# Performance work log

Hardware: AMD Instinct MI355X
Metric: run time of the kernel (lower is better)

## Reference

```python
import jax, jax.numpy as jnp
import numpy as np

EPS = 1e-6

def _ln(x, g, b):
    m = x.mean(-1, keepdims=True)
    v = jnp.var(x, axis=-1, keepdims=True)
    return (x - m) * jax.lax.rsqrt(v + EPS) * g + b

def _mha(x, qkv_w, out_w, out_b, heads, dh):
    # vit-style attention: Linear(dim, 3*heads*dh, bias=False), chunk into q,k,v
    B, N, _ = x.shape
    qkv = (x @ qkv_w).reshape(B, N, 3, heads, dh).transpose(2, 0, 3, 1, 4)
    q, k, v = qkv[0], qkv[1], qkv[2]                       # [B,H,N,dh]
    attn = jax.nn.softmax(jnp.einsum('bhid,bhjd->bhij', q, k) * (dh ** -0.5), axis=-1)
    o = jnp.einsum('bhij,bhjd->bhid', attn, v).transpose(0, 2, 1, 3).reshape(B, N, heads * dh)
    return o @ out_w + out_b

def _tx(x, p, heads, dh):
    # standard prenorm transformer stack, p = stacked per-layer params
    (l1g, l1b, qw, ow, ob, l2g, l2b, f1w, f1b, f2w, f2b, ng, nb) = p
    for i in range(l1g.shape[0]):
        x = x + _mha(_ln(x, l1g[i], l1b[i]), qw[i], ow[i], ob[i], heads, dh)
        h = _ln(x, l2g[i], l2b[i])
        x = x + jax.nn.gelu(h @ f1w[i] + f1b[i]) @ f2w[i] + f2b[i]
    return _ln(x, ng, nb)

def _ats(x, l1g, l1b, qkvw, qkvb, projw, projb, l2g, l2b, f1w, f1b, f2w, f2b):
    # ATS block: attention + CLS-significance-driven adaptive token resampling (gather)
    B, N, D = x.shape
    heads = 6
    dh = D // heads
    h = _ln(x, l1g, l1b)
    qkv = (h @ qkvw + qkvb).reshape(B, N, 3, heads, dh).transpose(2, 0, 3, 1, 4)
    q, k, v = qkv[0], qkv[1], qkv[2]
    attn = jax.nn.softmax(jnp.einsum('bhid,bhjd->bhij', q, k) * (dh ** -0.5), axis=-1)  # [B,H,N,N]
    y = jnp.einsum('bhij,bhjd->bhid', attn, v).transpose(0, 2, 1, 3).reshape(B, N, D)
    y = y @ projw + projb
    # significance score: cls attention * value norm (ATS, Fayyaz et al.)
    vn = jnp.linalg.norm(v, axis=-1)                        # [B,H,N]
    s = (attn[:, :, 0, 1:] * vn[:, :, 1:]).mean(axis=1)     # [B,N-1]
    s = s / (s.sum(-1, keepdims=True) + 1e-8)
    cdf = jnp.cumsum(s, axis=-1)                            # [B,N-1]
    # deterministic inverse-transform sampling of N-1 tokens
    u = (jnp.arange(N - 1, dtype=x.dtype) + 0.5) / (N - 1)
    idx = jax.vmap(lambda c: jnp.searchsorted(c, u))(cdf)
    idx = jnp.clip(idx, 0, N - 2) + 1                       # skip cls slot
    idx = jnp.concatenate([jnp.zeros((B, 1), idx.dtype), idx], axis=1)  # keep cls
    g = lambda a: jnp.take_along_axis(a, idx[:, :, None], axis=1)
    x = g(x) + g(y)
    h = _ln(x, l2g, l2b)
    return x + jax.nn.gelu(h @ f1w + f1b) @ f2w + f2b

def reference(x, patch_w, patch_b, pos_emb, space_token, temporal_token,
              s_ln1_g, s_ln1_b, s_qkv_w, s_out_w, s_out_b, s_ln2_g, s_ln2_b,
              s_fc1_w, s_fc1_b, s_fc2_w, s_fc2_b, s_norm_g, s_norm_b,
              t_ln1_g, t_ln1_b, t_qkv_w, t_out_w, t_out_b, t_ln2_g, t_ln2_b,
              t_fc1_w, t_fc1_b, t_fc2_w, t_fc2_b, t_norm_g, t_norm_b,
              a_ln1_g, a_ln1_b, a_qkv_w, a_qkv_b, a_proj_w, a_proj_b,
              a_ln2_g, a_ln2_b, a_fc1_w, a_fc1_b, a_fc2_w, a_fc2_b,
              final_g, final_b, h1_w, h1_b, h2_w, h2_b):
    B, T = x.shape[0], x.shape[1]
    BT, D, P, HP = B * T, 192, 16, 14
    # patch embedding (conv16s16 as unfold + linear), channel-major flattening
    xt = x.reshape(BT, 3, HP, P, HP, P).transpose(0, 2, 4, 1, 3, 5).reshape(BT, HP * HP, 3 * P * P)
    xt = (xt @ patch_w + patch_b).reshape(B, T, HP * HP, D)
    cls = jnp.broadcast_to(space_token.reshape(1, 1, 1, D), (B, T, 1, D))
    xt = jnp.concatenate([cls, xt], axis=2) + pos_emb      # [B,T,197,D]
    xt = xt.reshape(BT, 197, D)
    xt = _tx(xt, (s_ln1_g, s_ln1_b, s_qkv_w, s_out_w, s_out_b, s_ln2_g, s_ln2_b,
                  s_fc1_w, s_fc1_b, s_fc2_w, s_fc2_b, s_norm_g, s_norm_b), 6, 64)
    for i in range(a_ln1_g.shape[0]):
        xt = _ats(xt, a_ln1_g[i], a_ln1_b[i], a_qkv_w[i], a_qkv_b[i], a_proj_w[i],
                  a_proj_b[i], a_ln2_g[i], a_ln2_b[i], a_fc1_w[i], a_fc1_b[i],
                  a_fc2_w[i], a_fc2_b[i])
    xc = xt[:, 0].reshape(B, T, D)
    tt = jnp.broadcast_to(temporal_token, (B, 1, D))
    xc = jnp.concatenate([tt, xc], axis=1)                 # [B,T+1,D]
    xc = _tx(xc, (t_ln1_g, t_ln1_b, t_qkv_w, t_out_w, t_out_b, t_ln2_g, t_ln2_b,
                  t_fc1_w, t_fc1_b, t_fc2_w, t_fc2_b, t_norm_g, t_norm_b), 6, 64)
    f = jnp.max(xc, axis=1)                                # AdaptiveMaxPool1d(1) over tokens
    f = _ln(f, final_g, final_b)
    return jax.nn.relu(f @ h1_w + h1_b) @ h2_w + h2_b      # mlp_head -> [B,2]

def setup_inputs():
    key = jax.random.key(0)
    ks = iter(jax.random.split(key, 64))
    def rn(shape, s=0.02):
        return jax.random.normal(next(ks), shape, dtype=jnp.float32) * s
    d = {}
    d['x'] = jax.random.normal(next(ks), (16, 5, 3, 224, 224), dtype=jnp.float32)
    d['patch_w'] = rn((768, 192)); d['patch_b'] = jnp.zeros((192,), jnp.float32)
    d['pos_emb'] = rn((1, 5, 197, 192))
    d['space_token'] = rn((1, 1, 192)); d['temporal_token'] = rn((1, 1, 192))
    def tx(depth, n):
        d[n + '_ln1_g'] = jnp.ones((depth, 192), jnp.float32); d[n + '_ln1_b'] = jnp.zeros((depth, 192), jnp.float32)
        d[n + '_qkv_w'] = rn((depth, 192, 1152)); d[n + '_out_w'] = rn((depth, 384, 192)); d[n + '_out_b'] = jnp.zeros((depth, 192), jnp.float32)
        d[n + '_ln2_g'] = jnp.ones((depth, 192), jnp.float32); d[n + '_ln2_b'] = jnp.zeros((depth, 192), jnp.float32)
        d[n + '_fc1_w'] = rn((depth, 192, 768)); d[n + '_fc1_b'] = jnp.zeros((depth, 768), jnp.float32)
        d[n + '_fc2_w'] = rn((depth, 768, 192)); d[n + '_fc2_b'] = jnp.zeros((depth, 192), jnp.float32)
        d[n + '_norm_g'] = jnp.ones((192,), jnp.float32); d[n + '_norm_b'] = jnp.zeros((192,), jnp.float32)
    tx(2, 's'); tx(3, 't')
    d['a_ln1_g'] = jnp.ones((12, 192), jnp.float32); d['a_ln1_b'] = jnp.zeros((12, 192), jnp.float32)
    d['a_qkv_w'] = rn((12, 192, 576)); d['a_qkv_b'] = jnp.zeros((12, 576), jnp.float32)
    d['a_proj_w'] = rn((12, 192, 192)); d['a_proj_b'] = jnp.zeros((12, 192), jnp.float32)
    d['a_ln2_g'] = jnp.ones((12, 192), jnp.float32); d['a_ln2_b'] = jnp.zeros((12, 192), jnp.float32)
    d['a_fc1_w'] = rn((12, 192, 768)); d['a_fc1_b'] = jnp.zeros((12, 768), jnp.float32)
    d['a_fc2_w'] = rn((12, 768, 192)); d['a_fc2_b'] = jnp.zeros((12, 192), jnp.float32)
    d['final_g'] = jnp.ones((192,), jnp.float32); d['final_b'] = jnp.zeros((192,), jnp.float32)
    d['h1_w'] = rn((192, 64)); d['h1_b'] = jnp.zeros((64,), jnp.float32)
    d['h2_w'] = rn((64, 2)); d['h2_b'] = jnp.zeros((2,), jnp.float32)
    return d
```

## Files before the change

### kernel.cpp

```cpp
#include <hip/hip_runtime.h>
#include <hip/hip_bf16.h>
#include <math.h>

typedef float in_t;
typedef float out_t;

__device__ __forceinline__ float ldi(const in_t* p, size_t i) { return (float)p[i]; }

#define DMODEL 192
#define NTOK   197
#define BT_    80
#define ROWS_  (BT_*NTOK)

__device__ __forceinline__ float gelu_f(float v) {
  return 0.5f*v*(1.f + tanhf(0.7978845608028654f*(v + 0.044715f*v*v*v)));
}

__device__ __forceinline__ short f2bf(float f) {
  union { float f; unsigned u; } v; v.f = f;
  unsigned r = v.u + 0x7FFFu + ((v.u >> 16) & 1u);
  return (short)(r >> 16);
}

typedef __attribute__((ext_vector_type(8))) short bfrag;
typedef __attribute__((ext_vector_type(4))) float f32x4;

__global__ __launch_bounds__(256)
void wconv_k(const float* __restrict__ W, short* __restrict__ O, int K, int N)
{
  __shared__ float tile[32][33];
  const int l = blockIdx.z;
  const int k0 = blockIdx.y*32, n0 = blockIdx.x*32;
  const float* Wl = W + (size_t)l*K*N;
  short* Ol = O + (size_t)l*K*N;
  const int tx = threadIdx.x & 31, ty = threadIdx.x >> 5;
  #pragma unroll
  for (int r = ty; r < 32; r += 8) {
    int k = k0 + r, n = n0 + tx;
    tile[r][tx] = (k < K && n < N) ? Wl[(size_t)k*N + n] : 0.f;
  }
  __syncthreads();
  #pragma unroll
  for (int r = ty; r < 32; r += 8) {
    int n = n0 + r, k = k0 + tx;
    if (n < N && k < K) Ol[(size_t)n*K + k] = f2bf(tile[tx][r]);
  }
}

template<int EPI, int ABF, int OBF>
__global__ __launch_bounds__(256)
void gemmW_k(const void* __restrict__ Ain, const short* __restrict__ Wt,
             const float* __restrict__ bias, const float* __restrict__ R,
             void* __restrict__ Cout, float* __restrict__ Cout2,
             int M, int N, int K)
{
  constexpr int LP = 200;
  __shared__ short Asb[64][LP];
  __shared__ short Bsb[64][LP];
  const int t = threadIdx.x;
  const int w = t >> 6, lane = t & 63;
  const int bm0 = blockIdx.y*64, bn0 = blockIdx.x*64;
  const int sr = t >> 2;
  const int sk = (t & 3) * 8;
  f32x4 acc[4] = {};

  for (int k0 = 0; k0 < K; k0 += 192) {
    const int gm = bm0 + sr;
    #pragma unroll
    for (int cc = 0; cc < 6; ++cc) {
      const int kk = cc*32 + sk;
      short y[8] = {0,0,0,0,0,0,0,0};
      if (gm < M) {
        if (ABF == 0) {
          const float* ap = (const float*)Ain + (size_t)gm*K + k0 + kk;
          float4 v0 = *(const float4*)ap;
          float4 v1 = *(const float4*)(ap + 4);
          y[0]=f2bf(v0.x); y[1]=f2bf(v0.y); y[2]=f2bf(v0.z); y[3]=f2bf(v0.w);
          y[4]=f2bf(v1.x); y[5]=f2bf(v1.y); y[6]=f2bf(v1.z); y[7]=f2bf(v1.w);
        } else {
          *(bfrag*)y = *(const bfrag*)((const short*)Ain + (size_t)gm*K + k0 + kk);
        }
      }
      *(bfrag*)&Asb[sr][kk] = *(bfrag*)y;
      bfrag bv = *(const bfrag*)(Wt + (size_t)(bn0 + sr)*K + k0 + kk);
      *(bfrag*)&Bsb[sr][kk] = bv;
    }
    __syncthreads();
    const int fr = lane & 15, g8 = (lane >> 4) * 8;
    #pragma unroll
    for (int ks = 0; ks < 6; ++ks) {
      bfrag af = *(const bfrag*)&Asb[w*16 + fr][ks*32 + g8];
      #pragma unroll
      for (int nt = 0; nt < 4; ++nt) {
        bfrag bf = *(const bfrag*)&Bsb[nt*16 + fr][ks*32 + g8];
        acc[nt] = __builtin_amdgcn_mfma_f32_16x16x32_bf16(af, bf, acc[nt], 0, 0, 0);
      }
    }
    __syncthreads();
  }
  const int col = lane & 15, rg = (lane >> 4) * 4;
  #pragma unroll
  for (int nt = 0; nt < 4; ++nt) {
    int gn = bn0 + nt*16 + col;
    float bv = bias ? bias[gn] : 0.f;
    #pragma unroll
    for (int r = 0; r < 4; ++r) {
      int gm = bm0 + w*16 + rg + r;
      if (gm < M) {
        float v = acc[nt][r] + bv;
        if (EPI==1) v = gelu_f(v);
        if (EPI==2) v += R[(size_t)gm*N + gn];
        if (OBF==0)      ((float*)Cout)[(size_t)gm*N + gn] = v;
        else if (OBF==1) ((short*)Cout)[(size_t)gm*N + gn] = f2bf(v);
        else {
          if (gn < 384) ((short*)Cout)[(size_t)gm*384 + gn] = f2bf(v);
          else          Cout2[(size_t)gm*192 + (gn - 384)] = v;
        }
      }
    }
  }
}

__global__ __launch_bounds__(256)
void ln_k(const float* __restrict__ x, const in_t* __restrict__ g, const in_t* __restrict__ b,
          float* __restrict__ o, int rows)
{
  int t = threadIdx.x, wave = t>>6, lane = t&63;
  int r = blockIdx.x*4 + wave;
  if (r >= rows) return;
  const float* xr = x + (size_t)r*DMODEL;
  float e0 = xr[lane], e1 = xr[lane+64], e2 = xr[lane+128];
  float s = e0+e1+e2;
  #pragma unroll
  for (int off=32; off; off>>=1) s += __shfl_xor(s, off);
  float mean = s / 192.f;
  float d0=e0-mean, d1=e1-mean, d2=e2-mean;
  float v = d0*d0+d1*d1+d2*d2;
  #pragma unroll
  for (int off=32; off; off>>=1) v += __shfl_xor(v, off);
  float rs = 1.f / sqrtf(v/192.f + 1e-6f);
  float* orow = o + (size_t)r*DMODEL;
  orow[lane]     = d0*rs*ldi(g,lane)     + ldi(b,lane);
  orow[lane+64]  = d1*rs*ldi(g,lane+64)  + ldi(b,lane+64);
  orow[lane+128] = d2*rs*ldi(g,lane+128) + ldi(b,lane+128);
}

__global__ __launch_bounds__(256)
void gatherln_k(const float* __restrict__ X, const float* __restrict__ P,
                const int* __restrict__ idx, const in_t* __restrict__ g,
                const in_t* __restrict__ b, float* __restrict__ Xo,
                float* __restrict__ H2, int rows)
{
  int t = threadIdx.x, wave = t>>6, lane = t&63;
  int r = blockIdx.x*4 + wave;
  if (r >= rows) return;
  int bt = r / NTOK, n = r - bt*NTOK;
  int src = idx[(size_t)bt*NTOK + n];
  size_t sb = ((size_t)bt*NTOK + src)*DMODEL;
  float e0 = X[sb+lane]     + P[sb+lane];
  float e1 = X[sb+lane+64]  + P[sb+lane+64];
  float e2 = X[sb+lane+128] + P[sb+lane+128];
  float* xr = Xo + (size_t)r*DMODEL;
  xr[lane] = e0; xr[lane+64] = e1; xr[lane+128] = e2;
  float s = e0+e1+e2;
  #pragma unroll
  for (int off=32; off; off>>=1) s += __shfl_xor(s, off);
  float mean = s / 192.f;
  float d0=e0-mean, d1=e1-mean, d2=e2-mean;
  float v = d0*d0+d1*d1+d2*d2;
  #pragma unroll
  for (int off=32; off; off>>=1) v += __shfl_xor(v, off);
  float rs = 1.f / sqrtf(v/192.f + 1e-6f);
  float* orow = H2 + (size_t)r*DMODEL;
  orow[lane]     = d0*rs*ldi(g,lane)     + ldi(b,lane);
  orow[lane+64]  = d1*rs*ldi(g,lane+64)  + ldi(b,lane+64);
  orow[lane+128] = d2*rs*ldi(g,lane+128) + ldi(b,lane+128);
}

template<int DH, int W, int MODE>
__global__ __launch_bounds__(W*64)
void attnB_k(const short* __restrict__ qk, const float* __restrict__ vf,
             short* __restrict__ out, float* __restrict__ attn0,
             int heads, float scale)
{
  constexpr int NSEQ = 197;
  constexpr int NP   = 224;
  constexpr int KG   = DH/8;
  constexpr int CT   = DH/16;
  constexpr int NF   = DH/32;
  __shared__ short Kb[KG][NP][8];
  __shared__ short Vt[NP/8][DH][8];
  __shared__ short Ps[W][NP/8][16][8];

  const int bh = blockIdx.x;
  const int b = bh / heads, h = bh - b*heads;
  const int qks = ((MODE==1) ? 3 : 2)*heads*DH;
  const short* __restrict__ baseqk = qk + (size_t)b*NSEQ*qks;
  const int qo = h*DH, ko = heads*DH + h*DH;
  const int vs = heads*DH;
  const float* __restrict__ basev = (MODE==2) ? (vf + (size_t)b*NSEQ*vs) : nullptr;
  const int vo = (MODE==1) ? (2*heads*DH + h*DH) : (h*DH);
  const int t = threadIdx.x, w = t>>6, lane = t&63;

  {
    short z8[8] = {0,0,0,0,0,0,0,0};
    for (int idx = t; idx < NP*KG; idx += W*64) {
      int j = idx / KG, dg = idx - j*KG;
      bfrag kv = *(bfrag*)z8;
      if (j < NSEQ) kv = *(const bfrag*)(baseqk + (size_t)j*qks + ko + dg*8);
      *(bfrag*)&Kb[dg][j][0] = kv;
    }
  }
  for (int idx = t; idx < NP*DH; idx += W*64) {
    int j = idx / DH, d = idx - j*DH;
    short vv = 0;
    if (j < NSEQ) {
      if (MODE==1) vv = baseqk[(size_t)j*qks + vo + d];
      else         vv = f2bf(basev[(size_t)j*vs + vo + d]);
    }
    Vt[j>>3][d][j&7] = vv;
  }
  __syncthreads();

  const int c = lane & 15, g = lane >> 4, rg = g*4;
  const float NEG = -3.0e38f;

  for (int st = w; st < 13; st += W) {
    const int q0 = st*16;
    int qrow = q0 + c; if (qrow > NSEQ-1) qrow = NSEQ-1;
    bfrag aq[NF];
    {
      const short* qp = baseqk + (size_t)qrow*qks + qo + g*8;
      #pragma unroll
      for (int f = 0; f < NF; ++f) aq[f] = *(const bfrag*)(qp + f*32);
    }
    f32x4 sacc[14];
    #pragma unroll
    for (int jt = 0; jt < 14; ++jt) sacc[jt] = (f32x4){0.f,0.f,0.f,0.f};
    #pragma unroll
    for (int jt = 0; jt < 13; ++jt) {
      #pragma unroll
      for (int f = 0; f < NF; ++f) {
        bfrag bk = *(const bfrag*)&Kb[f*4 + g][jt*16 + c][0];
        sacc[jt] = __builtin_amdgcn_mfma_f32_16x16x32_bf16(aq[f], bk, sacc[jt], 0, 0, 0);
      }
    }
    float m0[4] = {NEG,NEG,NEG,NEG};
    #pragma unroll
    for (int jt = 0; jt < 14; ++jt) {
      const bool valid = (jt < 13) && (jt*16 + c < NSEQ);
      #pragma unroll
      for (int r = 0; r < 4; ++r) {
        float sv = valid ? sacc[jt][r]*scale : NEG;
        sacc[jt][r] = sv;
        m0[r] = fmaxf(m0[r], sv);
      }
    }
    #pragma unroll
    for (int off = 1; off < 16; off <<= 1)
      #pragma unroll
      for (int r = 0; r < 4; ++r) m0[r] = fmaxf(m0[r], __shfl_xor(m0[r], off));
    float sum[4] = {0.f,0.f,0.f,0.f};
    #pragma unroll
    for (int jt = 0; jt < 14; ++jt)
      #pragma unroll
      for (int r = 0; r < 4; ++r) {
        float e = expf(sacc[jt][r] - m0[r]);
        sacc[jt][r] = e;
        sum[r] += e;
      }
    #pragma unroll
    for (int off = 1; off < 16; off <<= 1)
      #pragma unroll
      for (int r = 0; r < 4; ++r) sum[r] += __shfl_xor(sum[r], off);
    float inv[4];
    #pragma unroll
    for (int r = 0; r < 4; ++r) inv[r] = 1.f / sum[r];

    if (attn0 != nullptr && st == 0 && g == 0) {
      #pragma unroll
      for (int jt = 0; jt < 13; ++jt) {
        int j = jt*16 + c;
        if (j < NSEQ) attn0[(size_t)bh*NSEQ + j] = sacc[jt][0]*inv[0];
      }
    }
    #pragma unroll
    for (int jt = 0; jt < 14; ++jt)
      #pragma unroll
      for (int r = 0; r < 4; ++r)
        Ps[w][jt*2 + (c>>3)][rg + r][c&7] = f2bf(sacc[jt][r]);
    f32x4 oacc[CT];
    #pragma unroll
    for (int ct = 0; ct < CT; ++ct) oacc[ct] = (f32x4){0.f,0.f,0.f,0.f};
    #pragma unroll
    for (int kc = 0; kc < 7; ++kc) {
      bfrag ap = *(const bfrag*)&Ps[w][kc*4 + g][c][0];
      #pragma unroll
      for (int ct = 0; ct < CT; ++ct) {
        bfrag bv = *(const bfrag*)&Vt[kc*4 + g][ct*16 + c][0];
        oacc[ct] = __builtin_amdgcn_mfma_f32_16x16x32_bf16(ap, bv, oacc[ct], 0, 0, 0);
      }
    }
    #pragma unroll
    for (int ct = 0; ct < CT; ++ct)
      #pragma unroll
      for (int r = 0; r < 4; ++r) {
        int q = q0 + rg + r;
        if (q < NSEQ)
          out[((size_t)b*NSEQ + q)*(size_t)(heads*DH) + h*DH + ct*16 + c] = f2bf(oacc[ct][r]*inv[r]);
      }
  }
}

template<int DH, int W>
__global__ __launch_bounds__(W*64)
void attn2r_k(const float* __restrict__ qkv, float* __restrict__ out,
              float* __restrict__ attn0, int Nseq, int heads, float scale)
{
  constexpr int QT = 8;
  constexpr int KTS = 204;
  constexpr int NPART = (DH == 64) ? 1 : 2;
  constexpr int DQ   = DH/4;
  constexpr int QPG  = 2;
  __shared__ float Kt[DH * KTS];
  __shared__ float Qt[W][DH][12];
  __shared__ float Ps[W][QT][200];

  const int bh = blockIdx.x;
  const int b = bh / heads, h = bh % heads;
  const int stride = 3 * heads * DH;
  const float* __restrict__ base = qkv + (size_t)b * Nseq * stride;
  const int qo = h * DH, ko = heads * DH + h * DH, vo = 2 * heads * DH + h * DH;
  const int t = threadIdx.x, w = t >> 6, lane = t & 63;

  for (int idx = t; idx < Nseq * DH; idx += W * 64) {
    int j = idx / DH, d0 = idx - j * DH;
    Kt[d0 * KTS + j] = base[(size_t)j * stride + ko + d0];
  }
  __syncthreads();

  const int d = lane & (DH - 1);
  const int nchunks = (Nseq + QT - 1) / QT;
  const int jcmax = (Nseq + 3) >> 2;
  const float NEG = -3.0e38f;
  const float4* Kt4 = (const float4*)Kt;

  const int part = (NPART == 2) ? (lane >> 5) : 0;
  const int qg   = (DH == 64) ? (lane >> 4) : ((lane >> 3) & 3);
  const int dq   = lane & (DQ - 1);
  const int dv   = 4 * dq;

  for (int ic = w; ic < nchunks; ic += W) {
    const int i0 = ic * QT;
    if ((DH == 64) || (lane >> 5) == 0) {
      #pragma unroll
      for (int q = 0; q < QT; ++q) {
        int i = i0 + q;
        Qt[w][d][q] = (i < Nseq) ? base[(size_t)i * stride + qo + d] : 0.f;
      }
    }
    float s[QT][4];
    #pragma unroll
    for (int q = 0; q < QT; ++q)
      #pragma unroll
      for (int u = 0; u < 4; ++u) s[q][u] = 0.f;
    #pragma unroll 4
    for (int dd = 0; dd < DH; ++dd) {
      float4 kv = (lane < 51) ? Kt4[dd * (KTS/4) + lane] : make_float4(0.f,0.f,0.f,0.f);
      float4 qA = *(const float4*)&Qt[w][dd][0];
      float4 qB = *(const float4*)&Qt[w][dd][4];
      float qv[8] = {qA.x, qA.y, qA.z, qA.w, qB.x, qB.y, qB.z, qB.w};
      float kr[4] = {kv.x, kv.y, kv.z, kv.w};
      #pragma unroll
      for (int q = 0; q < QT; ++q)
        #pragma unroll
        for (int u = 0; u < 4; ++u)
          s[q][u] = fmaf(qv[q], kr[u], s[q][u]);
    }
    float inv[QT];
    #pragma unroll
    for (int q = 0; q < QT; ++q) {
      float mx = NEG;
      #pragma unroll
      for (int u = 0; u < 4; ++u) {
        int j = 4*lane + u;
        s[q][u] = (j < Nseq) ? s[q][u]*scale : NEG;
        mx = fmaxf(mx, s[q][u]);
      }
      #pragma unroll
      for (int off = 32; off; off >>= 1) mx = fmaxf(mx, __shfl_xor(mx, off));
      float sum = 0.f;
      #pragma unroll
      for (int u = 0; u < 4; ++u) {
        float p = (4*lane + u < Nseq) ? expf(s[q][u] - mx) : 0.f;
        s[q][u] = p; sum += p;
      }
      #pragma unroll
      for (int off = 32; off; off >>= 1) sum += __shfl_xor(sum, off);
      inv[q] = 1.f / sum;
      if (lane < 50)
        *(float4*)&Ps[w][q][4*lane] = make_float4(s[q][0], s[q][1], s[q][2], s[q][3]);
    }
    if (attn0 != nullptr && i0 == 0) {
      #pragma unroll
      for (int u = 0; u < 4; ++u) {
        int j = 4*lane + u;
        if (j < Nseq) attn0[(size_t)bh*Nseq + j] = s[0][u]*inv[0];
      }
    }
    float o[QPG][4];
    #pragma unroll
    for (int qi = 0; qi < QPG; ++qi) { o[qi][0]=0.f; o[qi][1]=0.f; o[qi][2]=0.f; o[qi][3]=0.f; }
    const float* __restrict__ Vg = base + vo;
    for (int jc = part; jc < jcmax; jc += NPART) {
      const int jb = 4*jc;
      float4 V0 = make_float4(0.f,0.f,0.f,0.f), V1=V0, V2=V0, V3=V0;
      if (jb+0 < Nseq) V0 = *(const float4*)&Vg[(size_t)(jb+0)*stride + dv];
      if (jb+1 < Nseq) V1 = *(const float4*)&Vg[(size_t)(jb+1)*stride + dv];
      if (jb+2 < Nseq) V2 = *(const float4*)&Vg[(size_t)(jb+2)*stride + dv];
      if (jb+3 < Nseq) V3 = *(const float4*)&Vg[(size_t)(jb+3)*stride + dv];
      #pragma unroll
      for (int qi = 0; qi < QPG; ++qi) {
        float4 p4 = *(const float4*)&Ps[w][qg*QPG+qi][jb];
        o[qi][0] = fmaf(p4.w,V3.x, fmaf(p4.z,V2.x, fmaf(p4.y,V1.x, fmaf(p4.x,V0.x, o[qi][0]))));
        o[qi][1] = fmaf(p4.w,V3.y, fmaf(p4.z,V2.y, fmaf(p4.y,V1.y, fmaf(p4.x,V0.y, o[qi][1]))));
        o[qi][2] = fmaf(p4.w,V3.z, fmaf(p4.z,V2.z, fmaf(p4.y,V1.z, fmaf(p4.x,V0.z, o[qi][2]))));
        o[qi][3] = fmaf(p4.w,V3.w, fmaf(p4.z,V2.w, fmaf(p4.y,V1.w, fmaf(p4.x,V0.w, o[qi][3]))));
      }
    }
    if (NPART == 2) {
      #pragma unroll
      for (int qi = 0; qi < QPG; ++qi) {
        o[qi][0] += __shfl_xor(o[qi][0], 32);
        o[qi][1] += __shfl_xor(o[qi][1], 32);
        o[qi][2] += __shfl_xor(o[qi][2], 32);
        o[qi][3] += __shfl_xor(o[qi][3], 32);
      }
    }
    if (part == 0) {
      #pragma unroll
      for (int qi = 0; qi < QPG; ++qi) {
        float iv = inv[qi];
        if (qg == 1) iv = inv[QPG + qi];
        if (qg == 2) iv = inv[2*QPG + qi];
        if (qg == 3) iv = inv[3*QPG + qi];
        int i = i0 + qg*QPG + qi;
        if (i < Nseq) {
          float4 r = make_float4(o[qi][0]*iv, o[qi][1]*iv, o[qi][2]*iv, o[qi][3]*iv);
          *(float4*)&out[((size_t)b*Nseq + i)*(size_t)(heads*DH) + h*DH + dv] = r;
        }
      }
    }
  }
}

__global__ void patchify_k(const in_t* __restrict__ x, short* __restrict__ A)
{
  int idx = blockIdx.x*256 + threadIdx.x;
  const int total = BT_*196*768;
  if (idx >= total) return;
  int kc = idx % 768;
  int m  = idx / 768;
  int p  = m % 196;
  int bt = m / 196;
  int c  = kc >> 8;
  int py = (kc >> 4) & 15;
  int px = kc & 15;
  int ph = p / 14, pw = p % 14;
  size_t src = (((size_t)bt*3 + c)*224 + (ph*16+py))*224 + (pw*16+px);
  A[idx] = f2bf(ldi(x, src));
}

__global__ void assemble_k(const float* __restrict__ pt, const in_t* __restrict__ st,
                           const in_t* __restrict__ pe, float* __restrict__ X)
{
  int i = blockIdx.x*256 + threadIdx.x;
  const int total = BT_*NTOK*DMODEL;
  if (i >= total) return;
  int d  = i % DMODEL;
  int n  = (i / DMODEL) % NTOK;
  int bt = i / (DMODEL*NTOK);
  int tt = bt % 5;
  float base = (n == 0) ? ldi(st, d)
                        : pt[((size_t)bt*196 + (n-1))*DMODEL + d];
  X[i] = base + ldi(pe, ((size_t)tt*NTOK + n)*DMODEL + d);
}

__global__ __launch_bounds__(256)
void scoresample_k(const float* __restrict__ attn0, const float* __restrict__ Vf,
                   int* __restrict__ idxout)
{
  __shared__ float S[196];
  __shared__ float cdf[196];
  int b = blockIdx.x, t = threadIdx.x;
  if (t < 196) {
    int j = t + 1;
    float acc = 0.f;
    #pragma unroll
    for (int h = 0; h < 6; ++h) {
      float a0 = attn0[((size_t)b*6 + h)*NTOK + j];
      const float* v = Vf + ((size_t)b*NTOK + j)*192 + h*32;
      float ss = 0.f;
      #pragma unroll
      for (int d = 0; d < 32; ++d) ss += v[d]*v[d];
      acc += a0 * sqrtf(ss);
    }
    S[t] = acc / 6.0f;
  }
  __syncthreads();
  if (t == 0) {
    float tot = 0.f;
    for (int k = 0; k < 196; ++k) tot += S[k];
    float denom = tot + 1e-8f;
    float run = 0.f;
    for (int k = 0; k < 196; ++k) { run += S[k] / denom; cdf[k] = run; }
    idxout[(size_t)b*NTOK] = 0;
  }
  __syncthreads();
  if (t < 196) {
    float u = ((float)t + 0.5f) / 196.0f;
    int cnt = 0;
    for (int k = 0; k < 196; ++k) cnt += (cdf[k] < u) ? 1 : 0;
    int c = cnt > 195 ? 195 : cnt;
    idxout[(size_t)b*NTOK + 1 + t] = c + 1;
  }
}

__global__ void build_xc_k(const float* __restrict__ X, const in_t* __restrict__ tt,
                           float* __restrict__ xc)
{
  int i = blockIdx.x*256 + threadIdx.x;
  const int total = 16*6*DMODEL;
  if (i >= total) return;
  int d = i % DMODEL;
  int n = (i / DMODEL) % 6;
  int b = i / (DMODEL*6);
  xc[i] = (n == 0) ? ldi(tt, d)
                   : X[(((size_t)b*5 + (n-1))*NTOK + 0)*DMODEL + d];
}

__global__ __launch_bounds__(256)
void head_k(const float* __restrict__ xc, const in_t* __restrict__ fg, const in_t* __restrict__ fb,
            const in_t* __restrict__ w1, const in_t* __restrict__ b1,
            const in_t* __restrict__ w2, const in_t* __restrict__ b2,
            out_t* __restrict__ outp)
{
  __shared__ float fn[DMODEL];
  __shared__ float hid[64];
  __shared__ float mv[2];
  int b = blockIdx.x, t = threadIdx.x;
  if (t < DMODEL) {
    float m = xc[((size_t)b*6 + 0)*DMODEL + t];
    #pragma unroll
    for (int n = 1; n < 6; ++n) m = fmaxf(m, xc[((size_t)b*6 + n)*DMODEL + t]);
    fn[t] = m;
  }
  __syncthreads();
  if (t == 0) {
    float s = 0.f;
    for (int d = 0; d < DMODEL; ++d) s += fn[d];
    float mean = s / 192.f;
    float v = 0.f;
    for (int d = 0; d < DMODEL; ++d) { float dd = fn[d]-mean; v += dd*dd; }
    mv[0] = mean; mv[1] = 1.f / sqrtf(v/192.f + 1e-6f);
  }
  __syncthreads();
  if (t < DMODEL) fn[t] = (fn[t]-mv[0])*mv[1]*ldi(fg,t) + ldi(fb,t);
  __syncthreads();
  if (t < 64) {
    float a = ldi(b1, t);
    for (int d = 0; d < DMODEL; ++d) a += fn[d]*ldi(w1, (size_t)d*64 + t);
    hid[t] = fmaxf(a, 0.f);
  }
  __syncthreads();
  if (t < 2) {
    float a = ldi(b2, t);
    for (int j = 0; j < 64; ++j) a += hid[j]*ldi(w2, (size_t)j*2 + t);
    outp[(size_t)b*2 + t] = (out_t)a;
  }
}

extern "C" void kernel_launch(void* const* d_in, const int* in_sizes, int n_in,
                              void* d_out, int out_size, void* d_ws, size_t ws_size,
                              hipStream_t stream)
{
  if (n_in < 50) return;
  const in_t* x_in     = (const in_t*)d_in[0];
  const in_t* patch_w  = (const in_t*)d_in[1];
  const in_t* patch_b  = (const in_t*)d_in[2];
  const in_t* pos_emb  = (const in_t*)d_in[3];
  const in_t* space_tk = (const in_t*)d_in[4];
  const in_t* temp_tk  = (const in_t*)d_in[5];
  const in_t* s_ln1_g = (const in_t*)d_in[6];  const in_t* s_ln1_b = (const in_t*)d_in[7];
  const in_t* s_qkv_w = (const in_t*)d_in[8];  const in_t* s_out_w = (const in_t*)d_in[9];
  const in_t* s_out_b = (const in_t*)d_in[10]; const in_t* s_ln2_g = (const in_t*)d_in[11];
  const in_t* s_ln2_b = (const in_t*)d_in[12]; const in_t* s_fc1_w = (const in_t*)d_in[13];
  const in_t* s_fc1_b = (const in_t*)d_in[14]; const in_t* s_fc2_w = (const in_t*)d_in[15];
  const in_t* s_fc2_b = (const in_t*)d_in[16]; const in_t* s_nrm_g = (const in_t*)d_in[17];
  const in_t* s_nrm_b = (const in_t*)d_in[18];
  const in_t* t_ln1_g = (const in_t*)d_in[19]; const in_t* t_ln1_b = (const in_t*)d_in[20];
  const in_t* t_qkv_w = (const in_t*)d_in[21]; const in_t* t_out_w = (const in_t*)d_in[22];
  const in_t* t_out_b = (const in_t*)d_in[23]; const in_t* t_ln2_g = (const in_t*)d_in[24];
  const in_t* t_ln2_b = (const in_t*)d_in[25]; const in_t* t_fc1_w = (const in_t*)d_in[26];
  const in_t* t_fc1_b = (const in_t*)d_in[27]; const in_t* t_fc2_w = (const in_t*)d_in[28];
  const in_t* t_fc2_b = (const in_t*)d_in[29]; const in_t* t_nrm_g = (const in_t*)d_in[30];
  const in_t* t_nrm_b = (const in_t*)d_in[31];
  const in_t* a_ln1_g = (const in_t*)d_in[32]; const in_t* a_ln1_b = (const in_t*)d_in[33];
  const in_t* a_qkv_w = (const in_t*)d_in[34]; const in_t* a_qkv_b = (const in_t*)d_in[35];
  const in_t* a_prj_w = (const in_t*)d_in[36]; const in_t* a_prj_b = (const in_t*)d_in[37];
  const in_t* a_ln2_g = (const in_t*)d_in[38]; const in_t* a_ln2_b = (const in_t*)d_in[39];
  const in_t* a_fc1_w = (const in_t*)d_in[40]; const in_t* a_fc1_b = (const in_t*)d_in[41];
  const in_t* a_fc2_w = (const in_t*)d_in[42]; const in_t* a_fc2_b = (const in_t*)d_in[43];
  const in_t* final_g = (const in_t*)d_in[44]; const in_t* final_b = (const in_t*)d_in[45];
  const in_t* h1_w = (const in_t*)d_in[46];    const in_t* h1_b = (const in_t*)d_in[47];
  const in_t* h2_w = (const in_t*)d_in[48];    const in_t* h2_b = (const in_t*)d_in[49];

  float* ws = (float*)d_ws;
  size_t off = 0;
  auto alloc = [&](size_t nf) { size_t r = off; off += (nf + 63) & ~((size_t)63); return r; };
  size_t oX    = alloc((size_t)ROWS_*DMODEL);
  size_t oX2   = alloc((size_t)ROWS_*DMODEL);
  size_t oH    = alloc((size_t)ROWS_*DMODEL);
  size_t oH2   = alloc((size_t)ROWS_*DMODEL);
  size_t oY    = alloc((size_t)ROWS_*384);
  size_t oVf   = alloc((size_t)ROWS_*192);
  size_t oA0   = alloc((size_t)480*NTOK);
  size_t oXC   = alloc((size_t)16*6*DMODEL);
  size_t oIDX  = alloc((size_t)BT_*NTOK);
  size_t oQKVt = alloc((size_t)96*1152);
  size_t oFFt  = alloc((size_t)96*768);
  size_t oWB   = alloc((size_t)4202496 + 64);
  size_t oQKVb = alloc((size_t)ROWS_*1152/2 + 64);
  size_t oYb   = alloc((size_t)ROWS_*384/2 + 64);
  size_t oFFb  = alloc((size_t)ROWS_*768/2 + 64);
  if (ws_size < off*sizeof(float)) return;

  float* X    = ws + oX;
  float* X2   = ws + oX2;
  float* H    = ws + oH;
  float* H2   = ws + oH2;
  float* Y    = ws + oY;
  float* Vf   = ws + oVf;
  float* A0   = ws + oA0;
  float* XC   = ws + oXC;
  int*   IDX  = (int*)(ws + oIDX);
  float* QKVt = ws + oQKVt;
  float* FFt  = ws + oFFt;
  short* WB   = (short*)(ws + oWB);
  short* QKVb = (short*)(ws + oQKVb);
  short* Yb   = (short*)(ws + oYb);
  short* FFb  = (short*)(ws + oFFb);

  size_t wo = 0;
  auto wslot = [&](size_t n){ size_t r = wo; wo += n; return r; };
  size_t wPatch = wslot(147456);
  size_t wSqkv  = wslot(442368);
  size_t wSout  = wslot(147456);
  size_t wSfc1  = wslot(294912);
  size_t wSfc2  = wslot(294912);
  size_t wAqkv  = wslot(1327104);
  size_t wAprj  = wslot(442368);
  size_t wAfc1  = wslot(1769472);
  size_t wAfc2  = wslot(1769472);
  size_t wTqkv  = wslot(663552);
  size_t wTout  = wslot(221184);
  size_t wTfc1  = wslot(442368);
  size_t wTfc2  = wslot(442368);

  auto wconv = [&](const in_t* W, size_t slot, int K, int N, int L) {
    dim3 g(N/32, K/32, L);
    hipLaunchKernelGGL(wconv_k, g, dim3(256), 0, stream, W, WB + slot, K, N);
  };
  wconv(patch_w, wPatch, 768, 192, 1);
  wconv(s_qkv_w, wSqkv, 192, 1152, 2);
  wconv(s_out_w, wSout, 384, 192, 2);
  wconv(s_fc1_w, wSfc1, 192, 768, 2);
  wconv(s_fc2_w, wSfc2, 768, 192, 2);
  wconv(a_qkv_w, wAqkv, 192, 576, 12);
  wconv(a_prj_w, wAprj, 192, 192, 12);
  wconv(a_fc1_w, wAfc1, 192, 768, 12);
  wconv(a_fc2_w, wAfc2, 768, 192, 12);
  wconv(t_qkv_w, wTqkv, 192, 1152, 3);
  wconv(t_out_w, wTout, 384, 192, 3);
  wconv(t_fc1_w, wTfc1, 192, 768, 3);
  wconv(t_fc2_w, wTfc2, 768, 192, 3);

  auto gemm = [&](int epi, int abf, int obf, const void* A, const short* Wt,
                  const float* bias, const float* R, void* C, float* C2,
                  int M, int N, int K) {
    dim3 grid(N/64, (M+63)/64);
    if (obf==2)                        hipLaunchKernelGGL((gemmW_k<0,0,2>), grid, dim3(256), 0, stream, A, Wt, bias, R, C, C2, M, N, K);
    else if (epi==0 && abf==0 && obf==0) hipLaunchKernelGGL((gemmW_k<0,0,0>), grid, dim3(256), 0, stream, A, Wt, bias, R, C, C2, M, N, K);
    else if (epi==0 && abf==0 && obf==1) hipLaunchKernelGGL((gemmW_k<0,0,1>), grid, dim3(256), 0, stream, A, Wt, bias, R, C, C2, M, N, K);
    else if (epi==0 && abf==1 && obf==0) hipLaunchKernelGGL((gemmW_k<0,1,0>), grid, dim3(256), 0, stream, A, Wt, bias, R, C, C2, M, N, K);
    else if (epi==1 && obf==1)         hipLaunchKernelGGL((gemmW_k<1,0,1>), grid, dim3(256), 0, stream, A, Wt, bias, R, C, C2, M, N, K);
    else if (epi==1)                   hipLaunchKernelGGL((gemmW_k<1,0,0>), grid, dim3(256), 0, stream, A, Wt, bias, R, C, C2, M, N, K);
    else if (epi==2 && abf==1)         hipLaunchKernelGGL((gemmW_k<2,1,0>), grid, dim3(256), 0, stream, A, Wt, bias, R, C, C2, M, N, K);
    else                               hipLaunchKernelGGL((gemmW_k<2,0,0>), grid, dim3(256), 0, stream, A, Wt, bias, R, C, C2, M, N, K);
  };
  auto ln = [&](const float* xi, const in_t* g, const in_t* b, float* o, int rows) {
    hipLaunchKernelGGL(ln_k, dim3((rows+3)/4), dim3(256), 0, stream, xi, g, b, o, rows);
  };

  {
    int total = BT_*196*768;
    hipLaunchKernelGGL(patchify_k, dim3((total+255)/256), dim3(256), 0, stream, x_in, FFb);
    gemm(0, 1, 0, FFb, WB + wPatch, patch_b, nullptr, Y, nullptr, 15680, 192, 768);
    int tot2 = BT_*NTOK*DMODEL;
    hipLaunchKernelGGL(assemble_k, dim3((tot2+255)/256), dim3(256), 0, stream, Y, space_tk, pos_emb, X);
  }

  const float sc64 = 0.125f;
  const float sc32 = 0.17677669529663687f;

  for (int i = 0; i < 2; ++i) {
    ln(X, s_ln1_g + (size_t)i*192, s_ln1_b + (size_t)i*192, H, ROWS_);
    gemm(0, 0, 1, H, WB + wSqkv + (size_t)i*192*1152, nullptr, nullptr, QKVb, nullptr, ROWS_, 1152, 192);
    hipLaunchKernelGGL((attnB_k<64,8,1>), dim3(BT_*6), dim3(512), 0, stream, QKVb, (const float*)nullptr, Yb, (float*)nullptr, 6, sc64);
    gemm(2, 1, 0, Yb, WB + wSout + (size_t)i*384*192, s_out_b + (size_t)i*192, X, X, nullptr, ROWS_, 192, 384);
    ln(X, s_ln2_g + (size_t)i*192, s_ln2_b + (size_t)i*192, H, ROWS_);
    gemm(1, 0, 1, H, WB + wSfc1 + (size_t)i*192*768, s_fc1_b + (size_t)i*768, nullptr, FFb, nullptr, ROWS_, 768, 192);
    gemm(2, 1, 0, FFb, WB + wSfc2 + (size_t)i*768*192, s_fc2_b + (size_t)i*192, X, X, nullptr, ROWS_, 192, 768);
  }
  ln(X, s_nrm_g, s_nrm_b, X, ROWS_);

  float* xa = X; float* xb = X2;
  for (int i = 0; i < 12; ++i) {
    ln(xa, a_ln1_g + (size_t)i*192, a_ln1_b + (size_t)i*192, H, ROWS_);
    gemm(0, 0, 2, H, WB + wAqkv + (size_t)i*192*576, a_qkv_b + (size_t)i*576, nullptr, QKVb, Vf, ROWS_, 576, 192);
    hipLaunchKernelGGL((attnB_k<32,4,2>), dim3(BT_*6), dim3(256), 0, stream, QKVb, Vf, Yb, A0, 6, sc32);
    gemm(0, 1, 0, Yb, WB + wAprj + (size_t)i*192*192, a_prj_b + (size_t)i*192, nullptr, H, nullptr, ROWS_, 192, 192);
    hipLaunchKernelGGL(scoresample_k, dim3(BT_), dim3(256), 0, stream, A0, Vf, IDX);
    hipLaunchKernelGGL(gatherln_k, dim3((ROWS_+3)/4), dim3(256), 0, stream,
                       xa, H, IDX, a_ln2_g + (size_t)i*192, a_ln2_b + (size_t)i*192, xb, H2, ROWS_);
    gemm(1, 0, 1, H2, WB + wAfc1 + (size_t)i*192*768, a_fc1_b + (size_t)i*768, nullptr, FFb, nullptr, ROWS_, 768, 192);
    gemm(2, 1, 0, FFb, WB + wAfc2 + (size_t)i*768*192, a_fc2_b + (size_t)i*192, xb, xb, nullptr, ROWS_, 192, 768);
    float* tmp = xa; xa = xb; xb = tmp;
  }

  {
    int tot = 16*6*DMODEL;
    hipLaunchKernelGGL(build_xc_k, dim3((tot+255)/256), dim3(256), 0, stream, xa, temp_tk, XC);
  }
  const int MT = 16*6;
  for (int i = 0; i < 3; ++i) {
    ln(XC, t_ln1_g + (size_t)i*192, t_ln1_b + (size_t)i*192, H, MT);
    gemm(0, 0, 0, H, WB + wTqkv + (size_t)i*192*1152, nullptr, nullptr, QKVt, nullptr, MT, 1152, 192);
    hipLaunchKernelGGL((attn2r_k<64,8>), dim3(16*6), dim3(512), 0, stream, QKVt, Y, (float*)nullptr, 6, 6, sc64);
    gemm(2, 0, 0, Y, WB + wTout + (size_t)i*384*192, t_out_b + (size_t)i*192, XC, XC, nullptr, MT, 192, 384);
    ln(XC, t_ln2_g + (size_t)i*192, t_ln2_b + (size_t)i*192, H, MT);
    gemm(1, 0, 0, H, WB + wTfc1 + (size_t)i*192*768, t_fc1_b + (size_t)i*768, nullptr, FFt, nullptr, MT, 768, 192);
    gemm(2, 0, 0, FFt, WB + wTfc2 + (size_t)i*768*192, t_fc2_b + (size_t)i*192, XC, XC, nullptr, MT, 192, 768);
  }
  ln(XC, t_nrm_g, t_nrm_b, XC, MT);

  hipLaunchKernelGGL(head_k, dim3(16), dim3(256), 0, stream, XC, final_g, final_b,
                     h1_w, h1_b, h2_w, h2_b, (out_t*)d_out);
}
```

Measured before the change: 2.673 ms.

## Fuse FFN fc1+GELU+fc2 into a single kernel keeping hidden activations in LDS

Adds a fused MLP kernel. Each 64-row block computes fc1 with bias and GELU, keeps the 64x768 bf16 hidden tile in shared memory, then runs fc2 with bias and the residual add. It replaces the two GEMM launches in the spatial and ATS stacks, so the bf16 FF buffer is no longer written to and read back from global memory. In exchange it uses about 150KB of LDS per block, which allows roughly one block per CU. It also adds serialized per-chunk weight loads with no double buffering, and the grid shrinks to about 247 blocks.

New measurement: 2.663 ms. About the same (-0.4%).

```diff
diff --git a/kernel.cpp b/kernel.cpp
--- a/kernel.cpp
+++ b/kernel.cpp
@@ -115,6 +115,105 @@
         else {
           if (gn < 384) ((short*)Cout)[(size_t)gm*384 + gn] = f2bf(v);
           else          Cout2[(size_t)gm*192 + (gn - 384)] = v;
+        }
+      }
+    }
+  }
+}
+
+__global__ __launch_bounds__(256)
+void ffn_k(const float* __restrict__ Ain, const short* __restrict__ W1t,
+           const float* __restrict__ b1, const short* __restrict__ W2t,
+           const float* __restrict__ b2, const float* __restrict__ R,
+           float* __restrict__ Cout, int M)
+{
+  constexpr int LP = 200, FP = 776;
+  __shared__ short As[64][LP];
+  __shared__ short Bs[64][LP];
+  __shared__ short FF[64][FP];
+  const int t = threadIdx.x;
+  const int w = t >> 6, lane = t & 63;
+  const int bm0 = blockIdx.x*64;
+  const int sr = t >> 2;
+  const int sk = (t & 3) * 8;
+  const int fr = lane & 15, g8 = (lane >> 4) * 8;
+  const int col = lane & 15, rg = (lane >> 4) * 4;
+
+  {
+    const int gm = bm0 + sr;
+    #pragma unroll
+    for (int cc = 0; cc < 6; ++cc) {
+      const int kk = cc*32 + sk;
+      short y[8] = {0,0,0,0,0,0,0,0};
+      if (gm < M) {
+        const float* ap = Ain + (size_t)gm*192 + kk;
+        float4 v0 = *(const float4*)ap;
+        float4 v1 = *(const float4*)(ap + 4);
+        y[0]=f2bf(v0.x); y[1]=f2bf(v0.y); y[2]=f2bf(v0.z); y[3]=f2bf(v0.w);
+        y[4]=f2bf(v1.x); y[5]=f2bf(v1.y); y[6]=f2bf(v1.z); y[7]=f2bf(v1.w);
+      }
+      *(bfrag*)&As[sr][kk] = *(bfrag*)y;
+    }
+  }
+  for (int nc = 0; nc < 12; ++nc) {
+    #pragma unroll
+    for (int cc = 0; cc < 6; ++cc) {
+      const int kk = cc*32 + sk;
+      bfrag bv = *(const bfrag*)(W1t + (size_t)(nc*64 + sr)*192 + kk);
+      *(bfrag*)&Bs[sr][kk] = bv;
+    }
+    __syncthreads();
+    f32x4 acc[4] = {};
+    #pragma unroll
+    for (int ks = 0; ks < 6; ++ks) {
+      bfrag af = *(const bfrag*)&As[w*16 + fr][ks*32 + g8];
+      #pragma unroll
+      for (int nt = 0; nt < 4; ++nt) {
+        bfrag bf = *(const bfrag*)&Bs[nt*16 + fr][ks*32 + g8];
+        acc[nt] = __builtin_amdgcn_mfma_f32_16x16x32_bf16(af, bf, acc[nt], 0, 0, 0);
+      }
+    }
+    #pragma unroll
+    for (int nt = 0; nt < 4; ++nt) {
+      int gn = nc*64 + nt*16 + col;
+      float bv = b1[gn];
+      #pragma unroll
+      for (int r = 0; r < 4; ++r)
+        FF[w*16 + rg + r][gn] = f2bf(gelu_f(acc[nt][r] + bv));
+    }
+    __syncthreads();
+  }
+  for (int nc = 0; nc < 3; ++nc) {
+    f32x4 acc[4] = {};
+    for (int kc = 0; kc < 4; ++kc) {
+      #pragma unroll
+      for (int cc = 0; cc < 6; ++cc) {
+        const int kk = cc*32 + sk;
+        bfrag bv = *(const bfrag*)(W2t + (size_t)(nc*64 + sr)*768 + kc*192 + kk);
+        *(bfrag*)&Bs[sr][kk] = bv;
+      }
+      __syncthreads();
+      #pragma unroll
+      for (int ks = 0; ks < 6; ++ks) {
+        bfrag af = *(const bfrag*)&FF[w*16 + fr][kc*192 + ks*32 + g8];
+        #pragma unroll
+        for (int nt = 0; nt < 4; ++nt) {
+          bfrag bf = *(const bfrag*)&Bs[nt*16 + fr][ks*32 + g8];
+          acc[nt] = __builtin_amdgcn_mfma_f32_16x16x32_bf16(af, bf, acc[nt], 0, 0, 0);
+        }
+      }
+      __syncthreads();
+    }
+    #pragma unroll
+    for (int nt = 0; nt < 4; ++nt) {
+      int gn = nc*64 + nt*16 + col;
+      float bv = b2[gn];
+      #pragma unroll
+      for (int r = 0; r < 4; ++r) {
+        int gm = bm0 + w*16 + rg + r;
+        if (gm < M) {
+          float v = acc[nt][r] + bv + R[(size_t)gm*192 + gn];
+          Cout[(size_t)gm*192 + gn] = v;
         }
       }
     }
@@ -701,6 +800,11 @@
   auto ln = [&](const float* xi, const in_t* g, const in_t* b, float* o, int rows) {
     hipLaunchKernelGGL(ln_k, dim3((rows+3)/4), dim3(256), 0, stream, xi, g, b, o, rows);
   };
+  auto ffn = [&](const float* A, size_t w1, const float* b1, size_t w2, const float* b2,
+                 const float* R, float* C, int M) {
+    hipLaunchKernelGGL(ffn_k, dim3((M+63)/64), dim3(256), 0, stream,
+                       A, WB + w1, b1, WB + w2, b2, R, C, M);
+  };
 
   {
     int total = BT_*196*768;
@@ -719,8 +823,8 @@
     hipLaunchKernelGGL((attnB_k<64,8,1>), dim3(BT_*6), dim3(512), 0, stream, QKVb, (const float*)nullptr, Yb, (float*)nullptr, 6, sc64);
     gemm(2, 1, 0, Yb, WB + wSout + (size_t)i*384*192, s_out_b + (size_t)i*192, X, X, nullptr, ROWS_, 192, 384);
     ln(X, s_ln2_g + (size_t)i*192, s_ln2_b + (size_t)i*192, H, ROWS_);
-    gemm(1, 0, 1, H, WB + wSfc1 + (size_t)i*192*768, s_fc1_b + (size_t)i*768, nullptr, FFb, nullptr, ROWS_, 768, 192);
-    gemm(2, 1, 0, FFb, WB + wSfc2 + (size_t)i*768*192, s_fc2_b + (size_t)i*192, X, X, nullptr, ROWS_, 192, 768);
+    ffn(H, wSfc1 + (size_t)i*192*768, s_fc1_b + (size_t)i*768,
+        wSfc2 + (size_t)i*768*192, s_fc2_b + (size_t)i*192, X, X, ROWS_);
   }
   ln(X, s_nrm_g, s_nrm_b, X, ROWS_);
 
@@ -733,8 +837,8 @@
     hipLaunchKernelGGL(scoresample_k, dim3(BT_), dim3(256), 0, stream, A0, Vf, IDX);
     hipLaunchKernelGGL(gatherln_k, dim3((ROWS_+3)/4), dim3(256), 0, stream,
                        xa, H, IDX, a_ln2_g + (size_t)i*192, a_ln2_b + (size_t)i*192, xb, H2, ROWS_);
-    gemm(1, 0, 1, H2, WB + wAfc1 + (size_t)i*192*768, a_fc1_b + (size_t)i*768, nullptr, FFb, nullptr, ROWS_, 768, 192);
-    gemm(2, 1, 0, FFb, WB + wAfc2 + (size_t)i*768*192, a_fc2_b + (size_t)i*192, xb, xb, nullptr, ROWS_, 192, 768);
+    ffn(H2, wAfc1 + (size_t)i*192*768, a_fc1_b + (size_t)i*768,
+        wAfc2 + (size_t)i*768*192, a_fc2_b + (size_t)i*192, xb, xb, ROWS_);
     float* tmp = xa; xa = xb; xb = tmp;
   }
 
```
